# Optimization experiments

Hardware: AMD Instinct MI355X
Metric: run time of the kernel (lower is better)

The kernel has to match this reference:

```python
import jax, jax.numpy as jnp
import numpy as np

N_HEADS = 12
B, S, D = 2, 2048, 768
NEG = -1e9


def setup_inputs() -> dict:
    key = jax.random.key(0)
    ks = jax.random.split(key, 7)
    scale = 1.0 / np.sqrt(D)
    Q = jax.random.normal(ks[0], (B, S, D), jnp.float32)
    K = jax.random.normal(ks[1], (B, S, D), jnp.float32)
    V = jax.random.normal(ks[2], (B, S, D), jnp.float32)
    # causal mask, broadcastable over batch and heads; 0 entries are masked out
    mask = jnp.tril(jnp.ones((S, S), jnp.int32))[None, None, :, :]
    Wq = jax.random.normal(ks[3], (D, D), jnp.float32) * scale
    Wk = jax.random.normal(ks[4], (D, D), jnp.float32) * scale
    Wv = jax.random.normal(ks[5], (D, D), jnp.float32) * scale
    Wo = jax.random.normal(ks[6], (D, D), jnp.float32) * scale
    return {"Q": Q, "K": K, "V": V, "mask": mask,
            "Wq": Wq, "Wk": Wk, "Wv": Wv, "Wo": Wo}


def reference(Q, K, V, mask, Wq, Wk, Wv, Wo):
    b, s, d = Q.shape
    h = N_HEADS
    dk = d // h
    # projections (torch nn.Linear: x @ W.T), split heads -> (b, h, s, dk)
    q = (Q @ Wq.T).reshape(b, s, h, dk).transpose(0, 2, 1, 3)
    k = (K @ Wk.T).reshape(b, s, h, dk).transpose(0, 2, 1, 3)
    v = (V @ Wv.T).reshape(b, s, h, dk).transpose(0, 2, 1, 3)
    scores = jnp.einsum('bhqd,bhkd->bhqk', q, k) / jnp.sqrt(jnp.asarray(dk, q.dtype))
    scores = jnp.where(mask == 0, jnp.asarray(NEG, scores.dtype), scores)
    attn = jax.nn.softmax(scores, axis=-1)  # dropout p=0.0 -> identity
    ctx = jnp.einsum('bhqk,bhkd->bhqd', attn, v)
    ctx = ctx.transpose(0, 2, 1, 3).reshape(b, s, d)
    return ctx @ Wo.T
```

## Files before the change

### kernel.cpp

```cpp
#include <hip/hip_runtime.h>
#include <math.h>

#define NH     12
#define BB     2
#define SEQ    2048
#define DMODEL 768
#define DK     64

typedef __attribute__((ext_vector_type(8))) short short8;
typedef __attribute__((ext_vector_type(4))) short short4v;
typedef __attribute__((ext_vector_type(4))) float floatx4;

__device__ __forceinline__ unsigned short f2bf(float x) {
    unsigned u = __builtin_bit_cast(unsigned, x);
    u = (u + 0x7fffu + ((u >> 16) & 1u)) >> 16;
    return (unsigned short)u;
}
__device__ __forceinline__ unsigned short f2bf_fast(float x) {
    unsigned u = __builtin_bit_cast(unsigned, x);
    return (unsigned short)((u + 0x8000u) >> 16);
}
__device__ __forceinline__ float bf2f(unsigned short h) {
    unsigned u = ((unsigned)h) << 16;
    return __builtin_bit_cast(float, u);
}

__device__ __forceinline__ void gld_lds16(const ushort* gptr, ushort* lptr) {
    __builtin_amdgcn_global_load_lds(
        (const __attribute__((address_space(1))) unsigned int*)(const void*)gptr,
        (__attribute__((address_space(3))) unsigned int*)(void*)lptr,
        16, 0, 0);
}

__device__ __forceinline__ short4v shfl8(short4v v, int src) {
    int2 t = __builtin_bit_cast(int2, v);
    t.x = __shfl(t.x, src);
    t.y = __shfl(t.y, src);
    return __builtin_bit_cast(short4v, t);
}

#define SI (BB * SEQ * DMODEL)
#define SW (DMODEL * DMODEL)

#define P1_BLOCKS 1024

__global__ __launch_bounds__(256) void cast_w(
    const float* __restrict__ Wq, const float* __restrict__ Wk,
    const float* __restrict__ Wv, const float* __restrict__ Wo,
    ushort* oWq, ushort* oWk, ushort* oWv, ushort* oWo, int* counter) {
    if (blockIdx.x == 0 && threadIdx.x == 0) *counter = P1_BLOCKS;
    long i = (long)(blockIdx.x * 256 + threadIdx.x) * 4;
    const float* src; ushort* dst; long off;
    if      (i < 1L * SW) { src = Wq; dst = oWq; off = i; }
    else if (i < 2L * SW) { src = Wk; dst = oWk; off = i - 1L * SW; }
    else if (i < 3L * SW) { src = Wv; dst = oWv; off = i - 2L * SW; }
    else                  { src = Wo; dst = oWo; off = i - 3L * SW; }
    float4 v = *(const float4*)(src + off);
    ushort4 o;
    o.x = f2bf(v.x); o.y = f2bf(v.y); o.z = f2bf(v.z); o.w = f2bf(v.w);
    *(ushort4*)(dst + off) = o;
}

template<int MODE, bool AF32, int TM>
__device__ __forceinline__ void gemm_body(ushort* __restrict__ Sbase,
                                          const void* __restrict__ Av,
                                          const ushort* __restrict__ W,
                                          float* __restrict__ outF,
                                          ushort* __restrict__ outH,
                                          float scale) {
    constexpr int ATS = TM * 32;
    constexpr int BST = ATS + 128 * 32;
    constexpr int MI  = TM / 32;
    constexpr int AIT = TM / 64;
    constexpr int NWG = (TM == 128) ? 192 : 384;

    const int lin = blockIdx.y * 6 + blockIdx.x;
    const int swz = (lin & 7) * (NWG / 8) + (lin >> 3);
    const int n0 = (swz % 6) * 128;
    const int m0 = (swz / 6) * TM;

    const int tid  = threadIdx.x;
    const int lane = tid & 63;
    const int wv   = tid >> 6;
    const int l15  = lane & 15;
    const int quad = lane >> 4;
    const int wm = (wv >> 1) * (TM / 2);
    const int wn = (wv & 1) * 64;

    const int srow = tid >> 2;
    const int sch  = tid & 3;
    const int schx = sch ^ ((srow >> 1) & 3);
    const int sw2  = (l15 >> 1) & 3;

    const ushort* Ab = (const ushort*)Av;
    const float*  Af = (const float*)Av;

    floatx4 acc[MI][4];
    #pragma unroll
    for (int i = 0; i < MI; ++i)
        #pragma unroll
        for (int j = 0; j < 4; ++j) acc[i][j] = (floatx4)0.f;

    float4 ar0[2], ar1[2];
    #pragma unroll
    for (int it = 0; it < AIT; ++it) {
        const int r = srow + it * 64;
        if (AF32) {
            const float* p = Af + (size_t)(m0 + r) * DMODEL + schx * 8;
            ar0[it] = *(const float4*)p;
            ar1[it] = *(const float4*)(p + 4);
        } else {
            gld_lds16(Ab + (size_t)(m0 + r) * DMODEL + schx * 8, Sbase + r * 32 + sch * 8);
        }
    }
    #pragma unroll
    for (int it = 0; it < 2; ++it) {
        const int r = srow + it * 64;
        gld_lds16(W + (size_t)(n0 + r) * DMODEL + schx * 8, Sbase + ATS + r * 32 + sch * 8);
    }
    if (AF32) {
        #pragma unroll
        for (int it = 0; it < AIT; ++it) {
            const int r = srow + it * 64;
            short8 s8;
            s8[0] = (short)f2bf_fast(ar0[it].x); s8[1] = (short)f2bf_fast(ar0[it].y);
            s8[2] = (short)f2bf_fast(ar0[it].z); s8[3] = (short)f2bf_fast(ar0[it].w);
            s8[4] = (short)f2bf_fast(ar1[it].x); s8[5] = (short)f2bf_fast(ar1[it].y);
            s8[6] = (short)f2bf_fast(ar1[it].z); s8[7] = (short)f2bf_fast(ar1[it].w);
            *(short8*)(Sbase + r * 32 + sch * 8) = s8;
        }
    }

    const int NS = DMODEL / 32;
    for (int t = 0; t < NS; ++t) {
        __syncthreads();
        const int bi = (t + 1) & 1;
        ushort* SbufN = Sbase + bi * BST;
        if (t + 1 < NS) {
            const int k0 = (t + 1) * 32;
            #pragma unroll
            for (int it = 0; it < AIT; ++it) {
                const int r = srow + it * 64;
                if (AF32) {
                    const float* p = Af + (size_t)(m0 + r) * DMODEL + k0 + schx * 8;
                    ar0[it] = *(const float4*)p;
                    ar1[it] = *(const float4*)(p + 4);
                } else {
                    gld_lds16(Ab + (size_t)(m0 + r) * DMODEL + k0 + schx * 8, SbufN + r * 32 + sch * 8);
                }
            }
            #pragma unroll
            for (int it = 0; it < 2; ++it) {
                const int r = srow + it * 64;
                gld_lds16(W + (size_t)(n0 + r) * DMODEL + k0 + schx * 8, SbufN + ATS + r * 32 + sch * 8);
            }
        }
        const ushort* As  = Sbase + (t & 1) * BST;
        const ushort* Ws2 = As + ATS;
        short8 af[MI], bf[4];
        #pragma unroll
        for (int mi = 0; mi < MI; ++mi)
            af[mi] = *(const short8*)&As[(wm + mi * 16 + l15) * 32 + ((quad ^ sw2) * 8)];
        #pragma unroll
        for (int ni = 0; ni < 4; ++ni)
            bf[ni] = *(const short8*)&Ws2[(wn + ni * 16 + l15) * 32 + ((quad ^ sw2) * 8)];
        #pragma unroll
        for (int mi = 0; mi < MI; ++mi)
            #pragma unroll
            for (int ni = 0; ni < 4; ++ni) {
                if (MODE == 2)
                    acc[mi][ni] = __builtin_amdgcn_mfma_f32_16x16x32_bf16(bf[ni], af[mi], acc[mi][ni], 0, 0, 0);
                else
                    acc[mi][ni] = __builtin_amdgcn_mfma_f32_16x16x32_bf16(af[mi], bf[ni], acc[mi][ni], 0, 0, 0);
            }
        if (AF32 && t + 1 < NS) {
            #pragma unroll
            for (int it = 0; it < AIT; ++it) {
                const int r = srow + it * 64;
                short8 s8;
                s8[0] = (short)f2bf_fast(ar0[it].x); s8[1] = (short)f2bf_fast(ar0[it].y);
                s8[2] = (short)f2bf_fast(ar0[it].z); s8[3] = (short)f2bf_fast(ar0[it].w);
                s8[4] = (short)f2bf_fast(ar1[it].x); s8[5] = (short)f2bf_fast(ar1[it].y);
                s8[6] = (short)f2bf_fast(ar1[it].z); s8[7] = (short)f2bf_fast(ar1[it].w);
                *(short8*)(SbufN + r * 32 + sch * 8) = s8;
            }
        }
    }

    #pragma unroll
    for (int mi = 0; mi < MI; ++mi)
        #pragma unroll
        for (int ni = 0; ni < 4; ++ni)
            #pragma unroll
            for (int r = 0; r < 4; ++r) {
                const float v = acc[mi][ni][r] * scale;
                if (MODE == 2) {
                    const int m = m0 + wm + mi * 16 + l15;
                    const int n = n0 + wn + ni * 16 + quad * 4 + r;
                    const int b = m >> 11, s = m & (SEQ - 1);
                    const int h = n >> 6,  dk = n & 63;
                    outH[(((size_t)b * NH + h) * DK + dk) * SEQ + s] = f2bf(v);
                } else {
                    const int m = m0 + wm + mi * 16 + quad * 4 + r;
                    const int n = n0 + wn + ni * 16 + l15;
                    if (MODE == 0) {
                        outF[(size_t)m * DMODEL + n] = v;
                    } else {
                        const int b = m >> 11, s = m & (SEQ - 1);
                        const int h = n >> 6,  dk = n & 63;
                        outH[(((size_t)b * NH + h) * SEQ + s) * DK + dk] = f2bf(v);
                    }
                }
            }
}

#define QSCALE (0.125f * 1.44269504088896f)

__global__ __launch_bounds__(256) void gemm_qkv(
    const float* Q, const float* K, const float* V,
    const ushort* Wqb, const ushort* Wkb, const ushort* Wvb,
    ushort* qh, ushort* kh, ushort* vhT) {
    __shared__ __align__(16) ushort S[2 * (128 * 32 + 128 * 32)];
    const int z = blockIdx.z;
    if (z == 0)      gemm_body<1, true, 128>(S, Q, Wqb, nullptr, qh,  QSCALE);
    else if (z == 1) gemm_body<1, true, 128>(S, K, Wkb, nullptr, kh,  1.0f);
    else             gemm_body<2, true, 128>(S, V, Wvb, nullptr, vhT, 1.0f);
}

__global__ __launch_bounds__(256) void gemm_out(const ushort* A, const ushort* W, float* out) {
    __shared__ __align__(16) ushort S[2 * (64 * 32 + 128 * 32)];
    gemm_body<0, false, 64>(S, A, W, out, nullptr, 1.0f);
}

#define NIT   (24 * 72)
#define MBIAS -20.0f
__device__ const int d_offs[17] = {0,1,2,4,6,9,12,16,20,25,30,36,42,49,56,64,72};

__global__ __launch_bounds__(256, 4) void flash_p1(const ushort* __restrict__ qh,
                                                   const ushort* __restrict__ kh,
                                                   const ushort* __restrict__ vhT,
                                                   ushort* __restrict__ ctx,
                                                   ushort* __restrict__ Opart,
                                                   float* __restrict__ lpart,
                                                   int* __restrict__ counter) {
    const int tid  = threadIdx.x;
    const int lane = tid & 63;
    const int wv   = tid >> 6;
    const int l15  = lane & 15;
    const int quad = lane >> 4;

    __shared__ __align__(16) ushort KV[2][2][64 * 64];
    __shared__ int wshare;

    const int srow = tid >> 3;
    const int sch  = tid & 7;
    const int schx = sch ^ (srow & 7);
    const int swq  = l15 & 7;

    const int srcA = l15 + 32 * (quad & 1);
    const int srcB = srcA + 16;
    const bool hiq = (quad >> 1) != 0;

    const int colc[2] = { ((quad ^ swq) * 8), (((4 + quad) ^ swq) * 8) };

    int w = blockIdx.x;
    for (;;) {
        if (w >= NIT) break;
        if (tid == 0) wshare = atomicAdd(counter, 1);
        const int item = NIT - 1 - w;
        const int bh = item / 72;
        const int r72 = item - bh * 72;
        int Q = 0;
        #pragma unroll
        for (int q = 0; q < 16; ++q) if (r72 >= d_offs[q + 1]) Q = q + 1;
        const int s  = r72 - d_offs[Q];
        const int ns = (Q >> 1) + 1;
        const int b  = bh / NH, h = bh % NH;
        const int qbase = Q * 128;
        const int k_lo = 4 * s;
        const int k_hi = min(4 * s + 3, 2 * Q + 1);

        const ushort* kbase = kh  + (size_t)bh * SEQ * DK;
        const ushort* vbase = vhT + (size_t)bh * DK * SEQ;

        short8 qf[2][2];
        #pragma unroll
        for (int qs = 0; qs < 2; ++qs) {
            const ushort* qp = qh + ((size_t)bh * SEQ + qbase + wv * 32 + qs * 16 + l15) * DK;
            qf[qs][0] = *(const short8*)(qp + quad * 8);
            qf[qs][1] = *(const short8*)(qp + 32 + quad * 8);
        }

        {
            const int k0 = k_lo * 64;
            gld_lds16(kbase + (size_t)(k0 + srow) * DK + schx * 8,        &KV[0][0][srow * 64 + sch * 8]);
            gld_lds16(kbase + (size_t)(k0 + srow + 32) * DK + schx * 8,   &KV[0][0][(srow + 32) * 64 + sch * 8]);
            gld_lds16(vbase + (size_t)srow * SEQ + k0 + schx * 8,         &KV[0][1][srow * 64 + sch * 8]);
            gld_lds16(vbase + (size_t)(srow + 32) * SEQ + k0 + schx * 8,  &KV[0][1][(srow + 32) * 64 + sch * 8]);
        }

        float l_s[2] = {0.f, 0.f};
        floatx4 o_acc[2][4];
        #pragma unroll
        for (int qs = 0; qs < 2; ++qs)
            #pragma unroll
            for (int d = 0; d < 4; ++d) o_acc[qs][d] = (floatx4)0.f;

        for (int kt = k_lo; kt <= k_hi; ++kt) {
            __syncthreads();
            if (kt < k_hi) {
                const int k0 = (kt + 1) * 64;
                const int bi = (kt + 1 - k_lo) & 1;
                gld_lds16(kbase + (size_t)(k0 + srow) * DK + schx * 8,        &KV[bi][0][srow * 64 + sch * 8]);
                gld_lds16(kbase + (size_t)(k0 + srow + 32) * DK + schx * 8,   &KV[bi][0][(srow + 32) * 64 + sch * 8]);
                gld_lds16(vbase + (size_t)srow * SEQ + k0 + schx * 8,         &KV[bi][1][srow * 64 + sch * 8]);
                gld_lds16(vbase + (size_t)(srow + 32) * SEQ + k0 + schx * 8,  &KV[bi][1][(srow + 32) * 64 + sch * 8]);
            }
            const int cb = (kt - k_lo) & 1;
            const ushort* Ks  = KV[cb][0];
            const ushort* Vts = KV[cb][1];
            const bool diag = (kt >= 2 * Q);

            floatx4 s_acc[2][4];
            #pragma unroll
            for (int qs = 0; qs < 2; ++qs)
                #pragma unroll
                for (int nt = 0; nt < 4; ++nt) s_acc[qs][nt] = (floatx4)(MBIAS);
            #pragma unroll
            for (int kc = 0; kc < 2; ++kc)
                #pragma unroll
                for (int nt = 0; nt < 4; ++nt) {
                    short8 kf = *(const short8*)&Ks[(nt * 16 + l15) * 64 + colc[kc]];
                    s_acc[0][nt] = __builtin_amdgcn_mfma_f32_16x16x32_bf16(kf, qf[0][kc], s_acc[0][nt], 0, 0, 0);
                    s_acc[1][nt] = __builtin_amdgcn_mfma_f32_16x16x32_bf16(kf, qf[1][kc], s_acc[1][nt], 0, 0, 0);
                }

            if (diag) {
                #pragma unroll
                for (int qs = 0; qs < 2; ++qs) {
                    const int qg = qbase + wv * 32 + qs * 16 + l15;
                    #pragma unroll
                    for (int nt = 0; nt < 4; ++nt)
                        #pragma unroll
                        for (int rr = 0; rr < 4; ++rr)
                            if (kt * 64 + nt * 16 + quad * 4 + rr > qg) s_acc[qs][nt][rr] = -1.0e30f;
                }
            }

            short4v packed[2][4];
            #pragma unroll
            for (int qs = 0; qs < 2; ++qs) {
                float lp0 = 0.f, lp1 = 0.f, lp2 = 0.f, lp3 = 0.f;
                #pragma unroll
                for (int nt = 0; nt < 4; ++nt)
                    #pragma unroll
                    for (int rr = 0; rr < 4; ++rr) {
                        const float p = exp2f(s_acc[qs][nt][rr]);
                        if      (rr == 0) lp0 += p;
                        else if (rr == 1) lp1 += p;
                        else if (rr == 2) lp2 += p;
                        else              lp3 += p;
                        packed[qs][nt][rr] = (short)f2bf_fast(p);
                    }
                l_s[qs] += (lp0 + lp1) + (lp2 + lp3);
            }

            #pragma unroll
            for (int kc = 0; kc < 2; ++kc) {
                short8 pf[2];
                #pragma unroll
                for (int qs = 0; qs < 2; ++qs) {
                    short4v a0 = shfl8(packed[qs][2 * kc],     srcA);
                    short4v a1 = shfl8(packed[qs][2 * kc + 1], srcA);
                    short4v b0 = shfl8(packed[qs][2 * kc],     srcB);
                    short4v b1 = shfl8(packed[qs][2 * kc + 1], srcB);
                    short4v lo = hiq ? a1 : a0;
                    short4v hi = hiq ? b1 : b0;
                    pf[qs][0] = lo[0]; pf[qs][1] = lo[1]; pf[qs][2] = lo[2]; pf[qs][3] = lo[3];
                    pf[qs][4] = hi[0]; pf[qs][5] = hi[1]; pf[qs][6] = hi[2]; pf[qs][7] = hi[3];
                }
                #pragma unroll
                for (int dkt = 0; dkt < 4; ++dkt) {
                    short8 vf = *(const short8*)&Vts[(dkt * 16 + l15) * 64 + colc[kc]];
                    o_acc[0][dkt] = __builtin_amdgcn_mfma_f32_16x16x32_bf16(pf[0], vf, o_acc[0][dkt], 0, 0, 0);
                    o_acc[1][dkt] = __builtin_amdgcn_mfma_f32_16x16x32_bf16(pf[1], vf, o_acc[1][dkt], 0, 0, 0);
                }
            }
        }

        #pragma unroll
        for (int qs = 0; qs < 2; ++qs) {
            l_s[qs] += __shfl_xor(l_s[qs], 16);
            l_s[qs] += __shfl_xor(l_s[qs], 32);
        }

        if (ns == 1) {
            #pragma unroll
            for (int qs = 0; qs < 2; ++qs)
                #pragma unroll
                for (int rr = 0; rr < 4; ++rr) {
                    const float lr = __shfl(l_s[qs], quad * 20 + rr);
                    const float inv = 1.f / lr;
                    const int sg = qbase + wv * 32 + qs * 16 + quad * 4 + rr;
                    #pragma unroll
                    for (int dkt = 0; dkt < 4; ++dkt) {
                        const int d = h * DK + dkt * 16 + l15;
                        ctx[((size_t)b * SEQ + sg) * DMODEL + d] = f2bf(o_acc[qs][dkt][rr] * inv);
                    }
                }
        } else {
            const int pid = bh * 70 + (d_offs[Q] - 2) + s;
            ushort* op = Opart + (size_t)pid * (128 * 64);
            #pragma unroll
            for (int qs = 0; qs < 2; ++qs) {
                #pragma unroll
                for (int rr = 0; rr < 4; ++rr) {
                    const int row = wv * 32 + qs * 16 + quad * 4 + rr;
                    #pragma unroll
                    for (int dkt = 0; dkt < 4; ++dkt)
                        op[row * 64 + dkt * 16 + l15] = f2bf(o_acc[qs][dkt][rr]);
                }
                if (quad == 0)
                    lpart[(size_t)pid * 128 + wv * 32 + qs * 16 + l15] = l_s[qs];
            }
        }

        w = __builtin_amdgcn_readfirstlane(wshare);
        __syncthreads();
    }
}

__global__ __launch_bounds__(256) void flash_combine(const ushort* __restrict__ Opart,
                                                     const float* __restrict__ lpart,
                                                     ushort* __restrict__ ctx) {
    const int bh = blockIdx.x / 14;
    const int Q  = 2 + blockIdx.x % 14;
    const int ns = (Q >> 1) + 1;
    const int pbase = bh * 70 + (d_offs[Q] - 2);
    const int b = bh / NH, h = bh % NH;
    const int t = threadIdx.x;
    const int row = t >> 1;
    const int c0  = (t & 1) * 32;

    float lt = 0.f;
    for (int s2 = 0; s2 < ns; ++s2) lt += lpart[(size_t)(pbase + s2) * 128 + row];
    const float inv = 1.f / lt;

    float acc[32];
    #pragma unroll
    for (int j = 0; j < 32; ++j) acc[j] = 0.f;
    for (int s2 = 0; s2 < ns; ++s2) {
        const ushort* op = Opart + (size_t)(pbase + s2) * (128 * 64) + row * 64 + c0;
        #pragma unroll
        for (int j = 0; j < 32; j += 8) {
            short8 v = *(const short8*)(op + j);
            #pragma unroll
            for (int e = 0; e < 8; ++e) acc[j + e] += bf2f((unsigned short)v[e]);
        }
    }
    ushort* dst = ctx + ((size_t)b * SEQ + Q * 128 + row) * DMODEL + h * DK + c0;
    #pragma unroll
    for (int j = 0; j < 32; j += 8) {
        short8 o;
        #pragma unroll
        for (int e = 0; e < 8; ++e) o[e] = (short)f2bf(acc[j + e] * inv);
        *(short8*)(dst + j) = o;
    }
}

extern "C" void kernel_launch(void* const* d_in, const int* in_sizes, int n_in,
                              void* d_out, int out_size, void* d_ws, size_t ws_size,
                              hipStream_t stream) {
    const float* Q  = (const float*)d_in[0];
    const float* K  = (const float*)d_in[1];
    const float* V  = (const float*)d_in[2];
    const float* Wq = (const float*)d_in[4];
    const float* Wk = (const float*)d_in[5];
    const float* Wv = (const float*)d_in[6];
    const float* Wo = (const float*)d_in[7];

    char* ws = (char*)d_ws;
    const size_t SZ_IN = (size_t)SI * 2;
    const size_t SZ_W  = (size_t)SW * 2;
    ushort* Wqb   = (ushort*)(ws);
    ushort* Wkb   = (ushort*)(ws + SZ_W);
    ushort* Wvb   = (ushort*)(ws + 2 * SZ_W);
    ushort* Wob   = (ushort*)(ws + 3 * SZ_W);
    ushort* qh    = (ushort*)(ws + 4 * SZ_W);
    ushort* kh    = (ushort*)(ws + 4 * SZ_W + SZ_IN);
    ushort* vhT   = (ushort*)(ws + 4 * SZ_W + 2 * SZ_IN);
    ushort* ctx   = (ushort*)(ws + 4 * SZ_W + 3 * SZ_IN);
    ushort* Opart = (ushort*)(ws + 4 * SZ_W + 4 * SZ_IN);
    float*  lpart = (float*) (ws + 4 * SZ_W + 4 * SZ_IN + (size_t)1680 * 8192 * 2);
    int*    ctr   = (int*)   (ws + 4 * SZ_W + 4 * SZ_IN + (size_t)1680 * 8192 * 2
                                 + (size_t)1680 * 128 * 4);

    dim3 blk(256);
    cast_w<<<dim3(4 * SW / 1024), blk, 0, stream>>>(Wq, Wk, Wv, Wo,
                                                    Wqb, Wkb, Wvb, Wob, ctr);
    gemm_qkv<<<dim3(6, 32, 3), blk, 0, stream>>>(Q, K, V, Wqb, Wkb, Wvb, qh, kh, vhT);
    flash_p1<<<dim3(P1_BLOCKS), blk, 0, stream>>>(qh, kh, vhT, ctx, Opart, lpart, ctr);
    flash_combine<<<dim3(24 * 14), blk, 0, stream>>>(Opart, lpart, ctx);
    gemm_out<<<dim3(6, 64), blk, 0, stream>>>(ctx, Wob, (float*)d_out);
}
```

Measured before the change: 208.5 us.

## Pair adjacent query blocks per flash work item and drop atomic scheduler

Each flash_p1 block now handles two adjacent 128-row query blocks against the same 256-key chunk, so each K/V tile staged into LDS serves twice as many queries. The persistent atomic-counter work queue is replaced by a static grid of 864 blocks, with indices interleaved across eight groups to balance the uneven causal work. This roughly halves K/V global and LDS traffic per query and removes the atomic and its extra barrier. In exchange it doubles accumulator registers per thread, which may lower occupancy, and it gives up dynamic load balancing.

```diff
diff --git a/kernel.cpp b/kernel.cpp
--- a/kernel.cpp
+++ b/kernel.cpp
@@ -42,13 +42,10 @@
 #define SI (BB * SEQ * DMODEL)
 #define SW (DMODEL * DMODEL)
 
-#define P1_BLOCKS 1024
-
 __global__ __launch_bounds__(256) void cast_w(
     const float* __restrict__ Wq, const float* __restrict__ Wk,
     const float* __restrict__ Wv, const float* __restrict__ Wo,
-    ushort* oWq, ushort* oWk, ushort* oWv, ushort* oWo, int* counter) {
-    if (blockIdx.x == 0 && threadIdx.x == 0) *counter = P1_BLOCKS;
+    ushort* oWq, ushort* oWk, ushort* oWv, ushort* oWo) {
     long i = (long)(blockIdx.x * 256 + threadIdx.x) * 4;
     const float* src; ushort* dst; long off;
     if      (i < 1L * SW) { src = Wq; dst = oWq; off = i; }
@@ -232,7 +229,6 @@
     gemm_body<0, false, 64>(S, A, W, out, nullptr, 1.0f);
 }
 
-#define NIT   (24 * 72)
 #define MBIAS -20.0f
 __device__ const int d_offs[17] = {0,1,2,4,6,9,12,16,20,25,30,36,42,49,56,64,72};
 
@@ -241,8 +237,7 @@
                                                    const ushort* __restrict__ vhT,
                                                    ushort* __restrict__ ctx,
                                                    ushort* __restrict__ Opart,
-                                                   float* __restrict__ lpart,
-                                                   int* __restrict__ counter) {
+                                                   float* __restrict__ lpart) {
     const int tid  = threadIdx.x;
     const int lane = tid & 63;
     const int wv   = tid >> 6;
@@ -250,7 +245,6 @@
     const int quad = lane >> 4;
 
     __shared__ __align__(16) ushort KV[2][2][64 * 64];
-    __shared__ int wshare;
 
     const int srow = tid >> 3;
     const int sch  = tid & 7;
@@ -263,63 +257,64 @@
 
     const int colc[2] = { ((quad ^ swq) * 8), (((4 + quad) ^ swq) * 8) };
 
-    int w = blockIdx.x;
-    for (;;) {
-        if (w >= NIT) break;
-        if (tid == 0) wshare = atomicAdd(counter, 1);
-        const int item = NIT - 1 - w;
-        const int bh = item / 72;
-        const int r72 = item - bh * 72;
-        int Q = 0;
-        #pragma unroll
-        for (int q = 0; q < 16; ++q) if (r72 >= d_offs[q + 1]) Q = q + 1;
-        const int s  = r72 - d_offs[Q];
-        const int ns = (Q >> 1) + 1;
-        const int b  = bh / NH, h = bh % NH;
-        const int qbase = Q * 128;
-        const int k_lo = 4 * s;
-        const int k_hi = min(4 * s + 3, 2 * Q + 1);
-
-        const ushort* kbase = kh  + (size_t)bh * SEQ * DK;
-        const ushort* vbase = vhT + (size_t)bh * DK * SEQ;
-
-        short8 qf[2][2];
-        #pragma unroll
-        for (int qs = 0; qs < 2; ++qs) {
-            const ushort* qp = qh + ((size_t)bh * SEQ + qbase + wv * 32 + qs * 16 + l15) * DK;
-            qf[qs][0] = *(const short8*)(qp + quad * 8);
-            qf[qs][1] = *(const short8*)(qp + 32 + quad * 8);
-        }
-
-        {
-            const int k0 = k_lo * 64;
-            gld_lds16(kbase + (size_t)(k0 + srow) * DK + schx * 8,        &KV[0][0][srow * 64 + sch * 8]);
-            gld_lds16(kbase + (size_t)(k0 + srow + 32) * DK + schx * 8,   &KV[0][0][(srow + 32) * 64 + sch * 8]);
-            gld_lds16(vbase + (size_t)srow * SEQ + k0 + schx * 8,         &KV[0][1][srow * 64 + sch * 8]);
-            gld_lds16(vbase + (size_t)(srow + 32) * SEQ + k0 + schx * 8,  &KV[0][1][(srow + 32) * 64 + sch * 8]);
-        }
-
-        float l_s[2] = {0.f, 0.f};
-        floatx4 o_acc[2][4];
+    const int item = (blockIdx.x & 7) * 108 + (blockIdx.x >> 3);
+    const int bh  = item / 36;
+    const int r36 = item - bh * 36;
+    int p = 0;
+    #pragma unroll
+    for (int q = 0; q < 7; ++q) if (r36 >= ((q + 1) * (q + 2)) / 2) p = q + 1;
+    const int s = r36 - (p * (p + 1)) / 2;
+    const int b = bh / NH, h = bh % NH;
+    const int k_lo = 4 * s;
+    const int k_hi = 4 * s + 3;
+
+    const ushort* kbase = kh  + (size_t)bh * SEQ * DK;
+    const ushort* vbase = vhT + (size_t)bh * DK * SEQ;
+    const ushort* qrow  = qh + ((size_t)bh * SEQ + 2 * p * 128 + wv * 32 + l15) * DK;
+
+    {
+        const int k0 = k_lo * 64;
+        gld_lds16(kbase + (size_t)(k0 + srow) * DK + schx * 8,        &KV[0][0][srow * 64 + sch * 8]);
+        gld_lds16(kbase + (size_t)(k0 + srow + 32) * DK + schx * 8,   &KV[0][0][(srow + 32) * 64 + sch * 8]);
+        gld_lds16(vbase + (size_t)srow * SEQ + k0 + schx * 8,         &KV[0][1][srow * 64 + sch * 8]);
+        gld_lds16(vbase + (size_t)(srow + 32) * SEQ + k0 + schx * 8,  &KV[0][1][(srow + 32) * 64 + sch * 8]);
+    }
+
+    float l_s[2][2] = {{0.f, 0.f}, {0.f, 0.f}};
+    floatx4 o_acc[2][2][4];
+    #pragma unroll
+    for (int qb = 0; qb < 2; ++qb)
         #pragma unroll
         for (int qs = 0; qs < 2; ++qs)
             #pragma unroll
-            for (int d = 0; d < 4; ++d) o_acc[qs][d] = (floatx4)0.f;
-
-        for (int kt = k_lo; kt <= k_hi; ++kt) {
-            __syncthreads();
-            if (kt < k_hi) {
-                const int k0 = (kt + 1) * 64;
-                const int bi = (kt + 1 - k_lo) & 1;
-                gld_lds16(kbase + (size_t)(k0 + srow) * DK + schx * 8,        &KV[bi][0][srow * 64 + sch * 8]);
-                gld_lds16(kbase + (size_t)(k0 + srow + 32) * DK + schx * 8,   &KV[bi][0][(srow + 32) * 64 + sch * 8]);
-                gld_lds16(vbase + (size_t)srow * SEQ + k0 + schx * 8,         &KV[bi][1][srow * 64 + sch * 8]);
-                gld_lds16(vbase + (size_t)(srow + 32) * SEQ + k0 + schx * 8,  &KV[bi][1][(srow + 32) * 64 + sch * 8]);
-            }
-            const int cb = (kt - k_lo) & 1;
-            const ushort* Ks  = KV[cb][0];
-            const ushort* Vts = KV[cb][1];
-            const bool diag = (kt >= 2 * Q);
+            for (int d = 0; d < 4; ++d) o_acc[qb][qs][d] = (floatx4)0.f;
+
+    for (int kt = k_lo; kt <= k_hi; ++kt) {
+        __syncthreads();
+        if (kt < k_hi) {
+            const int k0 = (kt + 1) * 64;
+            const int bi = (kt + 1 - k_lo) & 1;
+            gld_lds16(kbase + (size_t)(k0 + srow) * DK + schx * 8,        &KV[bi][0][srow * 64 + sch * 8]);
+            gld_lds16(kbase + (size_t)(k0 + srow + 32) * DK + schx * 8,   &KV[bi][0][(srow + 32) * 64 + sch * 8]);
+            gld_lds16(vbase + (size_t)srow * SEQ + k0 + schx * 8,         &KV[bi][1][srow * 64 + sch * 8]);
+            gld_lds16(vbase + (size_t)(srow + 32) * SEQ + k0 + schx * 8,  &KV[bi][1][(srow + 32) * 64 + sch * 8]);
+        }
+        const int cb = (kt - k_lo) & 1;
+        const ushort* Ks  = KV[cb][0];
+        const ushort* Vts = KV[cb][1];
+
+        #pragma unroll
+        for (int qb = 0; qb < 2; ++qb) {
+            const int qbase = (2 * p + qb) * 128;
+            const bool diag = (kt >= 4 * p + 2 * qb);
+
+            short8 qf[2][2];
+            #pragma unroll
+            for (int qs = 0; qs < 2; ++qs) {
+                const ushort* qp = qrow + (size_t)(qb * 128 + qs * 16) * DK;
+                qf[qs][0] = *(const short8*)(qp + quad * 8);
+                qf[qs][1] = *(const short8*)(qp + 32 + quad * 8);
+            }
 
             floatx4 s_acc[2][4];
             #pragma unroll
@@ -355,14 +350,14 @@
                 for (int nt = 0; nt < 4; ++nt)
                     #pragma unroll
                     for (int rr = 0; rr < 4; ++rr) {
-                        const float p = exp2f(s_acc[qs][nt][rr]);
-                        if      (rr == 0) lp0 += p;
-                        else if (rr == 1) lp1 += p;
-                        else if (rr == 2) lp2 += p;
-                        else              lp3 += p;
-                        packed[qs][nt][rr] = (short)f2bf_fast(p);
+                        const float pe = exp2f(s_acc[qs][nt][rr]);
+                        if      (rr == 0) lp0 += pe;
+                        else if (rr == 1) lp1 += pe;
+                        else if (rr == 2) lp2 += pe;
+                        else              lp3 += pe;
+                        packed[qs][nt][rr] = (short)f2bf_fast(pe);
                     }
-                l_s[qs] += (lp0 + lp1) + (lp2 + lp3);
+                l_s[qb][qs] += (lp0 + lp1) + (lp2 + lp3);
             }
 
             #pragma unroll
@@ -382,33 +377,41 @@
                 #pragma unroll
                 for (int dkt = 0; dkt < 4; ++dkt) {
                     short8 vf = *(const short8*)&Vts[(dkt * 16 + l15) * 64 + colc[kc]];
-                    o_acc[0][dkt] = __builtin_amdgcn_mfma_f32_16x16x32_bf16(pf[0], vf, o_acc[0][dkt], 0, 0, 0);
-                    o_acc[1][dkt] = __builtin_amdgcn_mfma_f32_16x16x32_bf16(pf[1], vf, o_acc[1][dkt], 0, 0, 0);
-                }
-            }
-        }
-
+                    o_acc[qb][0][dkt] = __builtin_amdgcn_mfma_f32_16x16x32_bf16(pf[0], vf, o_acc[qb][0][dkt], 0, 0, 0);
+                    o_acc[qb][1][dkt] = __builtin_amdgcn_mfma_f32_16x16x32_bf16(pf[1], vf, o_acc[qb][1][dkt], 0, 0, 0);
+                }
+            }
+        }
+    }
+
+    #pragma unroll
+    for (int qb = 0; qb < 2; ++qb)
         #pragma unroll
         for (int qs = 0; qs < 2; ++qs) {
-            l_s[qs] += __shfl_xor(l_s[qs], 16);
-            l_s[qs] += __shfl_xor(l_s[qs], 32);
-        }
-
-        if (ns == 1) {
+            l_s[qb][qs] += __shfl_xor(l_s[qb][qs], 16);
+            l_s[qb][qs] += __shfl_xor(l_s[qb][qs], 32);
+        }
+
+    if (p == 0) {
+        #pragma unroll
+        for (int qb = 0; qb < 2; ++qb)
             #pragma unroll
             for (int qs = 0; qs < 2; ++qs)
                 #pragma unroll
                 for (int rr = 0; rr < 4; ++rr) {
-                    const float lr = __shfl(l_s[qs], quad * 20 + rr);
+                    const float lr = __shfl(l_s[qb][qs], quad * 20 + rr);
                     const float inv = 1.f / lr;
-                    const int sg = qbase + wv * 32 + qs * 16 + quad * 4 + rr;
+                    const int sg = qb * 128 + wv * 32 + qs * 16 + quad * 4 + rr;
                     #pragma unroll
                     for (int dkt = 0; dkt < 4; ++dkt) {
                         const int d = h * DK + dkt * 16 + l15;
-                        ctx[((size_t)b * SEQ + sg) * DMODEL + d] = f2bf(o_acc[qs][dkt][rr] * inv);
+                        ctx[((size_t)b * SEQ + sg) * DMODEL + d] = f2bf(o_acc[qb][qs][dkt][rr] * inv);
                     }
                 }
-        } else {
+    } else {
+        #pragma unroll
+        for (int qb = 0; qb < 2; ++qb) {
+            const int Q = 2 * p + qb;
             const int pid = bh * 70 + (d_offs[Q] - 2) + s;
             ushort* op = Opart + (size_t)pid * (128 * 64);
             #pragma unroll
@@ -418,15 +421,12 @@
                     const int row = wv * 32 + qs * 16 + quad * 4 + rr;
                     #pragma unroll
                     for (int dkt = 0; dkt < 4; ++dkt)
-                        op[row * 64 + dkt * 16 + l15] = f2bf(o_acc[qs][dkt][rr]);
+                        op[row * 64 + dkt * 16 + l15] = f2bf(o_acc[qb][qs][dkt][rr]);
                 }
                 if (quad == 0)
-                    lpart[(size_t)pid * 128 + wv * 32 + qs * 16 + l15] = l_s[qs];
-            }
-        }
-
-        w = __builtin_amdgcn_readfirstlane(wshare);
-        __syncthreads();
+                    lpart[(size_t)pid * 128 + wv * 32 + qs * 16 + l15] = l_s[qb][qs];
+            }
+        }
     }
 }
 
@@ -492,14 +492,12 @@
     ushort* ctx   = (ushort*)(ws + 4 * SZ_W + 3 * SZ_IN);
     ushort* Opart = (ushort*)(ws + 4 * SZ_W + 4 * SZ_IN);
     float*  lpart = (float*) (ws + 4 * SZ_W + 4 * SZ_IN + (size_t)1680 * 8192 * 2);
-    int*    ctr   = (int*)   (ws + 4 * SZ_W + 4 * SZ_IN + (size_t)1680 * 8192 * 2
-                                 + (size_t)1680 * 128 * 4);
 
     dim3 blk(256);
     cast_w<<<dim3(4 * SW / 1024), blk, 0, stream>>>(Wq, Wk, Wv, Wo,
-                                                    Wqb, Wkb, Wvb, Wob, ctr);
+                                                    Wqb, Wkb, Wvb, Wob);
     gemm_qkv<<<dim3(6, 32, 3), blk, 0, stream>>>(Q, K, V, Wqb, Wkb, Wvb, qh, kh, vhT);
-    flash_p1<<<dim3(P1_BLOCKS), blk, 0, stream>>>(qh, kh, vhT, ctx, Opart, lpart, ctr);
+    flash_p1<<<dim3(864), blk, 0, stream>>>(qh, kh, vhT, ctx, Opart, lpart);
     flash_combine<<<dim3(24 * 14), blk, 0, stream>>>(Opart, lpart, ctx);
     gemm_out<<<dim3(6, 64), blk, 0, stream>>>(ctx, Wob, (float*)d_out);
 }
```

New measurement: 261.1 us. 25.2% more time.
